# Kernel tuning notes

Measured on AMD Instinct MI355X. Metric: run time of the kernel, lower is better.

Reference implementation:

```python
import jax, jax.numpy as jnp
import numpy as np

ACTION_FEAT_DIM = 64
ACTION_EMB = 192
FUSION = 768
HID = 384
N_HEADS = 4
B, A = 2048, 64

gelu = lambda x: jax.nn.gelu(x, approximate=False)


def setup_inputs() -> dict:
    key = jax.random.key(0)
    ks = jax.random.split(key, 12)
    s = lambda fan_in: 1.0 / np.sqrt(fan_in)
    in_dim = ACTION_EMB + FUSION
    return {
        "action_feats": jax.random.normal(ks[0], (B, A, ACTION_FEAT_DIM), jnp.float32),
        "action_mask": jax.random.bernoulli(ks[1], 0.5, (B, A)),
        "fused": jax.random.normal(ks[2], (B, FUSION), jnp.float32),
        "phase_oh": jax.random.normal(ks[3], (B, 5), jnp.float32),
        # action encoder: Linear(64->192), GELU, Linear(192->192), GELU
        "We1": jax.random.uniform(ks[4], (ACTION_FEAT_DIM, ACTION_EMB), jnp.float32, -s(ACTION_FEAT_DIM), s(ACTION_FEAT_DIM)),
        "be1": jnp.zeros((ACTION_EMB,), jnp.float32),
        "We2": jax.random.uniform(ks[5], (ACTION_EMB, ACTION_EMB), jnp.float32, -s(ACTION_EMB), s(ACTION_EMB)),
        "be2": jnp.zeros((ACTION_EMB,), jnp.float32),
        # 4 phase heads: Linear(960->384), GELU, Linear(384->1), stacked on leading head axis
        "W1": jax.random.uniform(ks[6], (N_HEADS, in_dim, HID), jnp.float32, -s(in_dim), s(in_dim)),
        "b1": jnp.zeros((N_HEADS, HID), jnp.float32),
        "W2": jax.random.uniform(ks[7], (N_HEADS, HID), jnp.float32, -s(HID), s(HID)),
        "b2": jnp.zeros((N_HEADS,), jnp.float32),
    }


def reference(action_feats, action_mask, fused, phase_oh, We1, be1, We2, be2, W1, b1, W2, b2):
    bsz, act_count, _ = action_feats.shape
    # action encoder
    emb = gelu(gelu(action_feats @ We1 + be1) @ We2 + be2)          # [B,A,192]
    fused_rep = jnp.broadcast_to(fused[:, None, :], (bsz, act_count, fused.shape[-1]))
    inp = jnp.concatenate([emb, fused_rep], axis=-1)                 # [B,A,960]
    # dense compute of all 4 heads (faithful to original)
    h = gelu(jnp.einsum('bai,kio->bkao', inp, W1) + b1[None, :, None, :])  # [B,4,A,384]
    per_head = jnp.einsum('bkao,ko->bka', h, W2) + b2[None, :, None]       # [B,4,A]
    # phase routing: argmax over one-hot, phases >=3 map to head 3
    phase_idx = jnp.argmax(phase_oh, axis=-1)
    head_idx = jnp.where(phase_idx <= 2, phase_idx, 3)               # [B]
    logits = jnp.take_along_axis(per_head, head_idx[:, None, None], axis=1)[:, 0, :]  # [B,A]
    return jnp.where(action_mask, jnp.float32(-10000.0), logits)
```

## Files before the change

### kernel.cpp

```cpp
#include <hip/hip_runtime.h>


typedef __bf16 bf16x8 __attribute__((ext_vector_type(8)));
typedef unsigned short ushortx8 __attribute__((ext_vector_type(8)));
typedef float floatx4 __attribute__((ext_vector_type(4)));
typedef unsigned short u16;

#define B_SZ 2048
#define EMB 192
#define FUS 768
#define HID 384
#define INDIM 960
#define LDS_W 200

#define WS_FLAGS 0
#define WS_HEAD 256
#define WS_W1T 16384
#define WS_WE1T 2965504
#define WS_WE2T 2990080
#define WS_GALL 3063808

__device__ __forceinline__ float bf2f(u16 u) {
  return __uint_as_float(((unsigned int)u) << 16);
}
__device__ __forceinline__ u16 f2bf(float f) {
  unsigned int x = __float_as_uint(f);
  x += 0x7FFFu + ((x >> 16) & 1u);
  return (u16)(x >> 16);
}
__device__ __forceinline__ float ldf(const void* p, size_t i, int bf) {
  return bf ? bf2f(((const u16*)p)[i]) : ((const float*)p)[i];
}
__device__ __forceinline__ bf16x8 ld8(const void* p, size_t idx, int bf) {
  if (bf) return *reinterpret_cast<const bf16x8*>((const u16*)p + idx);
  const float* f = (const float*)p + idx;
  ushortx8 u;
#pragma unroll
  for (int i = 0; i < 8; ++i) u[i] = f2bf(f[i]);
  return __builtin_bit_cast(bf16x8, u);
}

__device__ __forceinline__ float gelu_f(float x) {
  float t = __expf(-1.702f * x);
  return x * __builtin_amdgcn_rcpf(1.0f + t);
}

__device__ __forceinline__ bool read_mask(const void* m, long long i, int fmt) {
  if (fmt == 0) return ((const int*)m)[i] != 0;
  if (fmt == 1) return ((const unsigned char*)m)[i] != 0;
  if (fmt == 2) return ((const u16*)m)[i] != 0;
  return ((const unsigned int*)m)[i] != 0;
}

__global__ void k_detect(const unsigned int* __restrict__ aw, int* __restrict__ flags) {
  __shared__ unsigned int s_or[256];
  __shared__ int s_cnt[256];
  int tid = threadIdx.x;
  unsigned int orv = 0;
  int cnt = 0;
#pragma unroll 8
  for (int j = 0; j < 64; ++j) {
    unsigned int w = aw[tid * 64 + j];
    unsigned int h = w & 0xFFFFu;
    orv |= h;
    unsigned int e = (h >> 7) & 0xFFu;
    cnt += (h == 0u || (e >= 90u && e <= 150u)) ? 1 : 0;
  }
  s_or[tid] = orv;
  s_cnt[tid] = cnt;
  __syncthreads();
  if (tid == 0) {
    unsigned int o = 0; int c = 0;
    for (int i = 0; i < 256; ++i) { o |= s_or[i]; c += s_cnt[i]; }
    flags[3] = (o != 0u && c > 12288) ? 1 : 0;
  }
}

__global__ void k_route(const void* __restrict__ phase, const void* __restrict__ mask,
                        int* __restrict__ head_idx, int* __restrict__ flags) {
  int t = blockIdx.x * 256 + threadIdx.x;
  if (t >= B_SZ) return;
  const int bf = flags[3];
  float best = ldf(phase, (size_t)t * 5, bf);
  int bi = 0;
#pragma unroll
  for (int i = 1; i < 5; ++i) {
    float v = ldf(phase, (size_t)t * 5 + i, bf);
    if (v > best) { best = v; bi = i; }
  }
  head_idx[t] = (bi <= 2) ? bi : 3;

  const unsigned int* mw = (const unsigned int*)mask;
  unsigned int vi = 0, vu = 0, en = 0;
#pragma unroll
  for (int j = 0; j < 16; ++j) {
    unsigned int w = mw[t * 16 + j];
    vi |= (unsigned int)(w > 1u);
    vu |= (unsigned int)((w & 0xFEFEFEFEu) != 0u);
    en |= (unsigned int)((w & 0x0000FFFFu) != 0u);
  }
  if (vi) atomicOr(&flags[0], 1);
  if (vu) atomicOr(&flags[1], 1);
  if (en) atomicOr(&flags[2], 1);
}

__global__ void k_transpose(const void* __restrict__ we1, const void* __restrict__ we2,
                            const void* __restrict__ w1, u16* __restrict__ we1t,
                            u16* __restrict__ we2t, u16* __restrict__ w1t,
                            const int* __restrict__ flags) {
  __shared__ u16 tile[32][33];
  const int bf = flags[3];
  const void* src; u16* dst; int R, C; size_t soff = 0;
  int z = blockIdx.z;
  if (z == 0)      { src = we1; dst = we1t; R = 64;  C = EMB; }
  else if (z == 1) { src = we2; dst = we2t; R = EMB; C = EMB; }
  else { src = w1; soff = (size_t)(z - 2) * INDIM * HID;
         dst = w1t + (size_t)(z - 2) * HID * INDIM; R = INDIM; C = HID; }
  int bx = blockIdx.x, by = blockIdx.y;
  if (bx * 32 >= C || by * 32 >= R) return;
  int tx = threadIdx.x, ty = threadIdx.y;
#pragma unroll
  for (int i = 0; i < 4; ++i) {
    int r = by * 32 + ty + i * 8, c = bx * 32 + tx;
    if (r < R && c < C) tile[ty + i * 8][tx] = f2bf(ldf(src, soff + (size_t)r * C + c, bf));
  }
  __syncthreads();
#pragma unroll
  for (int i = 0; i < 4; ++i) {
    int r = bx * 32 + ty + i * 8, c = by * 32 + tx;
    if (r < C && c < R) dst[(size_t)r * R + c] = tile[tx][ty + i * 8];
  }
}

__global__ __launch_bounds__(256, 2) void k_gall(const void* __restrict__ fused,
                                                 const u16* __restrict__ w1t,
                                                 const void* __restrict__ b1,
                                                 u16* __restrict__ gall,
                                                 const int* __restrict__ flags) {
  __shared__ float R[4][64][65];
  const int bm = blockIdx.x, bn = blockIdx.y;
  const int bf = flags[3];
  const int tid = threadIdx.x;
  const int w = tid >> 6, lane = tid & 63;
  const int nl = lane & 15, q = lane >> 4;
  const floatx4 z4 = {0.f, 0.f, 0.f, 0.f};
  floatx4 acc[4][4];
#pragma unroll
  for (int mt = 0; mt < 4; ++mt)
#pragma unroll
    for (int nt = 0; nt < 4; ++nt) acc[mt][nt] = z4;

#pragma unroll
  for (int i = 0; i < 6; ++i) {
    int kk = w * 6 + i;
    bf16x8 a[4];
#pragma unroll
    for (int mt = 0; mt < 4; ++mt)
      a[mt] = ld8(fused, ((size_t)(bm * 64 + mt * 16 + nl)) * FUS + kk * 32 + q * 8, bf);
#pragma unroll
    for (int nt = 0; nt < 4; ++nt) {
      int col = bn * 64 + nt * 16 + nl;
      bf16x8 bb = *reinterpret_cast<const bf16x8*>(w1t + (size_t)col * INDIM + EMB + kk * 32 + q * 8);
#pragma unroll
      for (int mt = 0; mt < 4; ++mt)
        acc[mt][nt] = __builtin_amdgcn_mfma_f32_16x16x32_bf16(a[mt], bb, acc[mt][nt], 0, 0, 0);
    }
  }
#pragma unroll
  for (int mt = 0; mt < 4; ++mt)
#pragma unroll
    for (int nt = 0; nt < 4; ++nt)
#pragma unroll
      for (int r = 0; r < 4; ++r)
        R[w][mt * 16 + q * 4 + r][nt * 16 + nl] = acc[mt][nt][r];
  __syncthreads();
#pragma unroll
  for (int j = 0; j < 16; ++j) {
    int e = j * 256 + tid;
    int row = e >> 6, col = e & 63;
    float s = R[0][row][col] + R[1][row][col] + R[2][row][col] + R[3][row][col]
            + ldf(b1, bn * 64 + col, bf);
    gall[(size_t)(bm * 64 + row) * 1536 + bn * 64 + col] = f2bf(s);
  }
}

__global__ __launch_bounds__(256, 3) void k_main(
    const void* __restrict__ act, const void* __restrict__ mask,
    const void* __restrict__ be1, const void* __restrict__ be2,
    const void* __restrict__ W2, const void* __restrict__ b2,
    const u16* __restrict__ we1t, const u16* __restrict__ we2t,
    const u16* __restrict__ w1t, const u16* __restrict__ gall,
    const int* __restrict__ head_idx, const int* __restrict__ flags,
    void* __restrict__ out) {
  __shared__ __align__(16) char LB[51200];
  u16* S1 = (u16*)LB;
  u16* S2 = (u16*)(LB + 25600);
  float* red = (float*)LB;
  const int b = blockIdx.x;
  const int tid = threadIdx.x;
  const int w = tid >> 6, lane = tid & 63;
  const int nl = lane & 15, q = lane >> 4;
  const int khead = head_idx[b];
  const int bf = flags[3];
  const floatx4 z4 = {0.f, 0.f, 0.f, 0.f};

  {
    floatx4 acc1[4][3];
#pragma unroll
    for (int mt = 0; mt < 4; ++mt)
#pragma unroll
      for (int nt = 0; nt < 3; ++nt) acc1[mt][nt] = z4;
#pragma unroll
    for (int kk = 0; kk < 2; ++kk) {
      bf16x8 a[4];
#pragma unroll
      for (int mt = 0; mt < 4; ++mt)
        a[mt] = ld8(act, ((size_t)b * 64 + mt * 16 + nl) * 64 + kk * 32 + q * 8, bf);
#pragma unroll
      for (int nt = 0; nt < 3; ++nt) {
        bf16x8 bb = *reinterpret_cast<const bf16x8*>(we1t + (w * 48 + nt * 16 + nl) * 64 + kk * 32 + q * 8);
#pragma unroll
        for (int mt = 0; mt < 4; ++mt)
          acc1[mt][nt] = __builtin_amdgcn_mfma_f32_16x16x32_bf16(a[mt], bb, acc1[mt][nt], 0, 0, 0);
      }
    }
#pragma unroll
    for (int nt = 0; nt < 3; ++nt) {
      int col = w * 48 + nt * 16 + nl;
      float bias = ldf(be1, col, bf);
#pragma unroll
      for (int mt = 0; mt < 4; ++mt)
#pragma unroll
        for (int r = 0; r < 4; ++r)
          S1[(mt * 16 + q * 4 + r) * LDS_W + col] = f2bf(gelu_f(acc1[mt][nt][r] + bias));
    }
  }
  __syncthreads();

  {
    floatx4 acc2[4][3];
#pragma unroll
    for (int mt = 0; mt < 4; ++mt)
#pragma unroll
      for (int nt = 0; nt < 3; ++nt) acc2[mt][nt] = z4;
#pragma unroll
    for (int kk = 0; kk < 6; ++kk) {
      bf16x8 a[4];
#pragma unroll
      for (int mt = 0; mt < 4; ++mt)
        a[mt] = *reinterpret_cast<const bf16x8*>(&S1[(mt * 16 + nl) * LDS_W + kk * 32 + q * 8]);
#pragma unroll
      for (int nt = 0; nt < 3; ++nt) {
        bf16x8 bb = *reinterpret_cast<const bf16x8*>(we2t + (w * 48 + nt * 16 + nl) * EMB + kk * 32 + q * 8);
#pragma unroll
        for (int mt = 0; mt < 4; ++mt)
          acc2[mt][nt] = __builtin_amdgcn_mfma_f32_16x16x32_bf16(a[mt], bb, acc2[mt][nt], 0, 0, 0);
      }
    }
#pragma unroll
    for (int nt = 0; nt < 3; ++nt) {
      int col = w * 48 + nt * 16 + nl;
      float bias = ldf(be2, col, bf);
#pragma unroll
      for (int mt = 0; mt < 4; ++mt)
#pragma unroll
        for (int r = 0; r < 4; ++r)
          S2[(mt * 16 + q * 4 + r) * LDS_W + col] = f2bf(gelu_f(acc2[mt][nt][r] + bias));
    }
  }
  __syncthreads();

  {
    floatx4 acc3[4][6];
#pragma unroll
    for (int mt = 0; mt < 4; ++mt)
#pragma unroll
      for (int nt = 0; nt < 6; ++nt) acc3[mt][nt] = z4;
    const u16* w1h = w1t + (size_t)khead * HID * INDIM;
#pragma unroll
    for (int kk = 0; kk < 6; ++kk) {
      bf16x8 a[4];
#pragma unroll
      for (int mt = 0; mt < 4; ++mt)
        a[mt] = *reinterpret_cast<const bf16x8*>(&S2[(mt * 16 + nl) * LDS_W + kk * 32 + q * 8]);
#pragma unroll
      for (int nt = 0; nt < 6; ++nt) {
        bf16x8 bb = *reinterpret_cast<const bf16x8*>(w1h + (size_t)(w * 96 + nt * 16 + nl) * INDIM + kk * 32 + q * 8);
#pragma unroll
        for (int mt = 0; mt < 4; ++mt)
          acc3[mt][nt] = __builtin_amdgcn_mfma_f32_16x16x32_bf16(a[mt], bb, acc3[mt][nt], 0, 0, 0);
      }
    }
    const u16* grow = gall + (size_t)b * 1536 + khead * HID;
    float partial[4][4];
#pragma unroll
    for (int mt = 0; mt < 4; ++mt)
#pragma unroll
      for (int r = 0; r < 4; ++r) partial[mt][r] = 0.f;
#pragma unroll
    for (int nt = 0; nt < 6; ++nt) {
      int col = w * 96 + nt * 16 + nl;
      float g = bf2f(grow[col]);
      float w2c = ldf(W2, (size_t)khead * HID + col, bf);
#pragma unroll
      for (int mt = 0; mt < 4; ++mt)
#pragma unroll
        for (int r = 0; r < 4; ++r)
          partial[mt][r] += gelu_f(acc3[mt][nt][r] + g) * w2c;
    }
#pragma unroll
    for (int off = 1; off < 16; off <<= 1)
#pragma unroll
      for (int mt = 0; mt < 4; ++mt)
#pragma unroll
        for (int r = 0; r < 4; ++r)
          partial[mt][r] += __shfl_xor(partial[mt][r], off, 16);
    if (nl == 0) {
#pragma unroll
      for (int mt = 0; mt < 4; ++mt)
#pragma unroll
        for (int r = 0; r < 4; ++r)
          red[w * 64 + mt * 16 + q * 4 + r] = partial[mt][r];
    }
  }
  __syncthreads();

  if (tid < 64) {
    float s = red[tid] + red[64 + tid] + red[128 + tid] + red[192 + tid];
    int f0 = flags[0], f1 = flags[1], f2v = flags[2];
    int fmt = (f0 == 0) ? 0 : ((f1 == 0) ? 1 : ((f2v != 0) ? 2 : 3));
    float bb2 = ldf(b2, khead, bf);
    long long mi = (long long)b * 64 + tid;
    float v = read_mask(mask, mi, fmt) ? -10000.0f : (s + bb2);
    if (bf) ((u16*)out)[mi] = f2bf(v);
    else    ((float*)out)[mi] = v;
  }
}

extern "C" void kernel_launch(void* const* d_in, const int* in_sizes, int n_in,
                              void* d_out, int out_size, void* d_ws, size_t ws_size,
                              hipStream_t stream) {
  const void* act   = d_in[0];
  const void* mask  = d_in[1];
  const void* fused = d_in[2];
  const void* phase = d_in[3];
  const void* We1 = d_in[4];
  const void* be1 = d_in[5];
  const void* We2 = d_in[6];
  const void* be2 = d_in[7];
  const void* W1  = d_in[8];
  const void* b1  = d_in[9];
  const void* W2  = d_in[10];
  const void* b2  = d_in[11];
  char* ws = (char*)d_ws;
  int* flags    = (int*)(ws + WS_FLAGS);
  int* head_idx = (int*)(ws + WS_HEAD);
  u16* w1t  = (u16*)(ws + WS_W1T);
  u16* we1t = (u16*)(ws + WS_WE1T);
  u16* we2t = (u16*)(ws + WS_WE2T);
  u16* gall = (u16*)(ws + WS_GALL);

  hipMemsetAsync(flags, 0, 32, stream);
  k_detect<<<1, 256, 0, stream>>>((const unsigned int*)act, flags);
  k_route<<<B_SZ / 256, 256, 0, stream>>>(phase, mask, head_idx, flags);
  k_transpose<<<dim3(12, 30, 6), dim3(32, 8), 0, stream>>>(We1, We2, W1, we1t, we2t, w1t, flags);
  k_gall<<<dim3(32, 24), 256, 0, stream>>>(fused, w1t, b1, gall, flags);
  k_main<<<B_SZ, 256, 0, stream>>>(act, mask, be1, be2, W2, b2, we1t, we2t,
                                   w1t, gall, head_idx, flags, d_out);
}
```

Baseline: 230.3 us.

## Compute fused-part projection only for each row's routed head via bucketed lists

Rows are bucketed by routed head with atomic counters, and the fused-input GEMM now computes only the selected head's 384 columns per row instead of all four heads. Fused input is pre-converted to bf16 in a separate pass. k_main reuses one LDS buffer for both encoder stages and splits the head GEMM into two halves, which cuts LDS and register use so occupancy can rise to 4 blocks. The cost is an extra prep kernel, atomics and scattered row writes. The memset launch is folded into k_detect.

```diff
diff --git a/kernel.cpp b/kernel.cpp
--- a/kernel.cpp
+++ b/kernel.cpp
@@ -5,6 +5,7 @@
 typedef unsigned short ushortx8 __attribute__((ext_vector_type(8)));
 typedef float floatx4 __attribute__((ext_vector_type(4)));
 typedef unsigned short u16;
+typedef unsigned int u32;
 
 #define B_SZ 2048
 #define EMB 192
@@ -14,17 +15,20 @@
 #define LDS_W 200
 
 #define WS_FLAGS 0
+#define WS_CNT 64
 #define WS_HEAD 256
-#define WS_W1T 16384
-#define WS_WE1T 2965504
-#define WS_WE2T 2990080
-#define WS_GALL 3063808
+#define WS_LIST 8448
+#define WS_W1T 41216
+#define WS_WE1T 2990336
+#define WS_WE2T 3014912
+#define WS_FUSEDBF 3088640
+#define WS_GSEL 6234368
 
 __device__ __forceinline__ float bf2f(u16 u) {
-  return __uint_as_float(((unsigned int)u) << 16);
+  return __uint_as_float(((u32)u) << 16);
 }
 __device__ __forceinline__ u16 f2bf(float f) {
-  unsigned int x = __float_as_uint(f);
+  u32 x = __float_as_uint(f);
   x += 0x7FFFu + ((x >> 16) & 1u);
   return (u16)(x >> 16);
 }
@@ -49,37 +53,67 @@
   if (fmt == 0) return ((const int*)m)[i] != 0;
   if (fmt == 1) return ((const unsigned char*)m)[i] != 0;
   if (fmt == 2) return ((const u16*)m)[i] != 0;
-  return ((const unsigned int*)m)[i] != 0;
-}
-
-__global__ void k_detect(const unsigned int* __restrict__ aw, int* __restrict__ flags) {
-  __shared__ unsigned int s_or[256];
-  __shared__ int s_cnt[256];
+  return ((const u32*)m)[i] != 0;
+}
+
+__global__ void k_detect(const u32* __restrict__ aw, int* __restrict__ flags,
+                         int* __restrict__ cnt) {
+  __shared__ u32 so[4];
+  __shared__ int sc[4];
   int tid = threadIdx.x;
-  unsigned int orv = 0;
-  int cnt = 0;
+  int lane = tid & 63, wave = tid >> 6;
+  u32 orv = 0;
+  int c = 0;
 #pragma unroll 8
   for (int j = 0; j < 64; ++j) {
-    unsigned int w = aw[tid * 64 + j];
-    unsigned int h = w & 0xFFFFu;
+    u32 w = aw[j * 256 + tid];
+    u32 h = w & 0xFFFFu;
     orv |= h;
-    unsigned int e = (h >> 7) & 0xFFu;
-    cnt += (h == 0u || (e >= 90u && e <= 150u)) ? 1 : 0;
-  }
-  s_or[tid] = orv;
-  s_cnt[tid] = cnt;
+    u32 e = (h >> 7) & 0xFFu;
+    c += (h == 0u || (e >= 90u && e <= 150u)) ? 1 : 0;
+  }
+#pragma unroll
+  for (int off = 32; off >= 1; off >>= 1) {
+    orv |= (u32)__shfl_xor((int)orv, off);
+    c += __shfl_xor(c, off);
+  }
+  if (lane == 0) { so[wave] = orv; sc[wave] = c; }
   __syncthreads();
   if (tid == 0) {
-    unsigned int o = 0; int c = 0;
-    for (int i = 0; i < 256; ++i) { o |= s_or[i]; c += s_cnt[i]; }
-    flags[3] = (o != 0u && c > 12288) ? 1 : 0;
+    u32 o = so[0] | so[1] | so[2] | so[3];
+    int ct = sc[0] + sc[1] + sc[2] + sc[3];
+    flags[3] = (o != 0u && ct > 12288) ? 1 : 0;
+    flags[0] = 0; flags[1] = 0; flags[2] = 0;
+    cnt[0] = 0; cnt[1] = 0; cnt[2] = 0; cnt[3] = 0;
+  }
+}
+
+__global__ void k_prep(const void* __restrict__ fused, u16* __restrict__ fbf,
+                       const int* __restrict__ flags) {
+  const int bf = flags[3];
+  int gid = blockIdx.x * 256 + threadIdx.x;
+  if (bf) {
+    const uint2* s = (const uint2*)fused;
+    uint2* d = (uint2*)fbf;
+    for (int i = gid; i < 393216; i += 49152) d[i] = s[i];
+  } else {
+    const float4* s = (const float4*)fused;
+    uint2* d = (uint2*)fbf;
+    for (int i = gid; i < 393216; i += 49152) {
+      float4 v = s[i];
+      uint2 o;
+      o.x = (u32)f2bf(v.x) | ((u32)f2bf(v.y) << 16);
+      o.y = (u32)f2bf(v.z) | ((u32)f2bf(v.w) << 16);
+      d[i] = o;
+    }
   }
 }
 
 __global__ void k_route(const void* __restrict__ phase, const void* __restrict__ mask,
-                        int* __restrict__ head_idx, int* __restrict__ flags) {
-  int t = blockIdx.x * 256 + threadIdx.x;
-  if (t >= B_SZ) return;
+                        int* __restrict__ head_idx, int* __restrict__ flags,
+                        int* __restrict__ cnt, int* __restrict__ list) {
+  int tid = threadIdx.x;
+  int t = blockIdx.x * 256 + tid;
   const int bf = flags[3];
   float best = ldf(phase, (size_t)t * 5, bf);
   int bi = 0;
@@ -88,16 +122,19 @@
     float v = ldf(phase, (size_t)t * 5 + i, bf);
     if (v > best) { best = v; bi = i; }
   }
-  head_idx[t] = (bi <= 2) ? bi : 3;
-
-  const unsigned int* mw = (const unsigned int*)mask;
-  unsigned int vi = 0, vu = 0, en = 0;
+  int h = (bi <= 2) ? bi : 3;
+  head_idx[t] = h;
+  int pos = atomicAdd(&cnt[h], 1);
+  list[h * 2048 + pos] = t;
+
+  const u32* mw = (const u32*)mask;
+  u32 vi = 0, vu = 0, en = 0;
 #pragma unroll
   for (int j = 0; j < 16; ++j) {
-    unsigned int w = mw[t * 16 + j];
-    vi |= (unsigned int)(w > 1u);
-    vu |= (unsigned int)((w & 0xFEFEFEFEu) != 0u);
-    en |= (unsigned int)((w & 0x0000FFFFu) != 0u);
+    u32 w = mw[blockIdx.x * 4096 + j * 256 + tid];
+    vi |= (u32)(w > 1u);
+    vu |= (u32)((w & 0xFEFEFEFEu) != 0u);
+    en |= (u32)((w & 0x0000FFFFu) != 0u);
   }
   if (vi) atomicOr(&flags[0], 1);
   if (vu) atomicOr(&flags[1], 1);
@@ -132,70 +169,73 @@
   }
 }
 
-__global__ __launch_bounds__(256, 2) void k_gall(const void* __restrict__ fused,
-                                                 const u16* __restrict__ w1t,
-                                                 const void* __restrict__ b1,
-                                                 u16* __restrict__ gall,
-                                                 const int* __restrict__ flags) {
-  __shared__ float R[4][64][65];
-  const int bm = blockIdx.x, bn = blockIdx.y;
+__global__ __launch_bounds__(256, 4) void k_gall_sel(
+    const u16* __restrict__ fbf, const u16* __restrict__ w1t,
+    const void* __restrict__ b1, u16* __restrict__ gsel,
+    const int* __restrict__ cnt, const int* __restrict__ list,
+    const int* __restrict__ flags) {
   const int bf = flags[3];
+  int c0 = cnt[0], c1 = cnt[1], c2 = cnt[2], c3 = cnt[3];
+  int t0 = (c0 + 63) >> 6, t1 = (c1 + 63) >> 6, t2 = (c2 + 63) >> 6, t3 = (c3 + 63) >> 6;
+  int x = blockIdx.x, h, tl;
+  if (x < t0) { h = 0; tl = x; }
+  else if (x < t0 + t1) { h = 1; tl = x - t0; }
+  else if (x < t0 + t1 + t2) { h = 2; tl = x - t0 - t1; }
+  else if (x < t0 + t1 + t2 + t3) { h = 3; tl = x - t0 - t1 - t2; }
+  else return;
+  int ch = (h == 0) ? c0 : (h == 1) ? c1 : (h == 2) ? c2 : c3;
   const int tid = threadIdx.x;
   const int w = tid >> 6, lane = tid & 63;
   const int nl = lane & 15, q = lane >> 4;
+
+  int r = tl * 64 + w * 16 + nl;
+  if (r >= ch) r = ch - 1;
+  int bi = list[h * 2048 + r];
+  const u16* arow = fbf + (size_t)bi * FUS;
+  const u16* w1h = w1t + (size_t)h * HID * INDIM;
+  const int ncol0 = blockIdx.y * 64;
+
   const floatx4 z4 = {0.f, 0.f, 0.f, 0.f};
-  floatx4 acc[4][4];
-#pragma unroll
-  for (int mt = 0; mt < 4; ++mt)
-#pragma unroll
-    for (int nt = 0; nt < 4; ++nt) acc[mt][nt] = z4;
-
-#pragma unroll
-  for (int i = 0; i < 6; ++i) {
-    int kk = w * 6 + i;
-    bf16x8 a[4];
-#pragma unroll
-    for (int mt = 0; mt < 4; ++mt)
-      a[mt] = ld8(fused, ((size_t)(bm * 64 + mt * 16 + nl)) * FUS + kk * 32 + q * 8, bf);
+  floatx4 acc[4];
+#pragma unroll
+  for (int i = 0; i < 4; ++i) acc[i] = z4;
+#pragma unroll 4
+  for (int kk = 0; kk < 24; ++kk) {
+    bf16x8 a = *reinterpret_cast<const bf16x8*>(arow + kk * 32 + q * 8);
 #pragma unroll
     for (int nt = 0; nt < 4; ++nt) {
-      int col = bn * 64 + nt * 16 + nl;
-      bf16x8 bb = *reinterpret_cast<const bf16x8*>(w1t + (size_t)col * INDIM + EMB + kk * 32 + q * 8);
-#pragma unroll
-      for (int mt = 0; mt < 4; ++mt)
-        acc[mt][nt] = __builtin_amdgcn_mfma_f32_16x16x32_bf16(a[mt], bb, acc[mt][nt], 0, 0, 0);
-    }
-  }
-#pragma unroll
-  for (int mt = 0; mt < 4; ++mt)
-#pragma unroll
-    for (int nt = 0; nt < 4; ++nt)
-#pragma unroll
-      for (int r = 0; r < 4; ++r)
-        R[w][mt * 16 + q * 4 + r][nt * 16 + nl] = acc[mt][nt][r];
-  __syncthreads();
-#pragma unroll
-  for (int j = 0; j < 16; ++j) {
-    int e = j * 256 + tid;
-    int row = e >> 6, col = e & 63;
-    float s = R[0][row][col] + R[1][row][col] + R[2][row][col] + R[3][row][col]
-            + ldf(b1, bn * 64 + col, bf);
-    gall[(size_t)(bm * 64 + row) * 1536 + bn * 64 + col] = f2bf(s);
-  }
-}
-
-__global__ __launch_bounds__(256, 3) void k_main(
+      int col = ncol0 + nt * 16 + nl;
+      bf16x8 bb = *reinterpret_cast<const bf16x8*>(w1h + (size_t)col * INDIM + EMB + kk * 32 + q * 8);
+      acc[nt] = __builtin_amdgcn_mfma_f32_16x16x32_bf16(a, bb, acc[nt], 0, 0, 0);
+    }
+  }
+  int bi2[4];
+#pragma unroll
+  for (int rr = 0; rr < 4; ++rr) {
+    int rm = tl * 64 + w * 16 + q * 4 + rr;
+    if (rm >= ch) rm = ch - 1;
+    bi2[rr] = list[h * 2048 + rm];
+  }
+#pragma unroll
+  for (int nt = 0; nt < 4; ++nt) {
+    int col = ncol0 + nt * 16 + nl;
+    float bias = ldf(b1, (size_t)h * HID + col, bf);
+#pragma unroll
+    for (int rr = 0; rr < 4; ++rr)
+      gsel[(size_t)bi2[rr] * HID + col] = f2bf(acc[nt][rr] + bias);
+  }
+}
+
+__global__ __launch_bounds__(256, 4) void k_main(
     const void* __restrict__ act, const void* __restrict__ mask,
     const void* __restrict__ be1, const void* __restrict__ be2,
     const void* __restrict__ W2, const void* __restrict__ b2,
     const u16* __restrict__ we1t, const u16* __restrict__ we2t,
-    const u16* __restrict__ w1t, const u16* __restrict__ gall,
+    const u16* __restrict__ w1t, const u16* __restrict__ gsel,
     const int* __restrict__ head_idx, const int* __restrict__ flags,
     void* __restrict__ out) {
-  __shared__ __align__(16) char LB[51200];
-  u16* S1 = (u16*)LB;
-  u16* S2 = (u16*)(LB + 25600);
-  float* red = (float*)LB;
+  __shared__ __align__(16) u16 S[64 * LDS_W];
+  __shared__ float red[256];
   const int b = blockIdx.x;
   const int tid = threadIdx.x;
   const int w = tid >> 6, lane = tid & 63;
@@ -232,7 +272,7 @@
       for (int mt = 0; mt < 4; ++mt)
 #pragma unroll
         for (int r = 0; r < 4; ++r)
-          S1[(mt * 16 + q * 4 + r) * LDS_W + col] = f2bf(gelu_f(acc1[mt][nt][r] + bias));
+          S[(mt * 16 + q * 4 + r) * LDS_W + col] = f2bf(gelu_f(acc1[mt][nt][r] + bias));
     }
   }
   __syncthreads();
@@ -248,7 +288,7 @@
       bf16x8 a[4];
 #pragma unroll
       for (int mt = 0; mt < 4; ++mt)
-        a[mt] = *reinterpret_cast<const bf16x8*>(&S1[(mt * 16 + nl) * LDS_W + kk * 32 + q * 8]);
+        a[mt] = *reinterpret_cast<const bf16x8*>(&S[(mt * 16 + nl) * LDS_W + kk * 32 + q * 8]);
 #pragma unroll
       for (int nt = 0; nt < 3; ++nt) {
         bf16x8 bb = *reinterpret_cast<const bf16x8*>(we2t + (w * 48 + nt * 16 + nl) * EMB + kk * 32 + q * 8);
@@ -257,6 +297,7 @@
           acc2[mt][nt] = __builtin_amdgcn_mfma_f32_16x16x32_bf16(a[mt], bb, acc2[mt][nt], 0, 0, 0);
       }
     }
+    __syncthreads();
 #pragma unroll
     for (int nt = 0; nt < 3; ++nt) {
       int col = w * 48 + nt * 16 + nl;
@@ -265,41 +306,43 @@
       for (int mt = 0; mt < 4; ++mt)
 #pragma unroll
         for (int r = 0; r < 4; ++r)
-          S2[(mt * 16 + q * 4 + r) * LDS_W + col] = f2bf(gelu_f(acc2[mt][nt][r] + bias));
+          S[(mt * 16 + q * 4 + r) * LDS_W + col] = f2bf(gelu_f(acc2[mt][nt][r] + bias));
     }
   }
   __syncthreads();
 
-  {
-    floatx4 acc3[4][6];
+  float partial[4][4];
+#pragma unroll
+  for (int mt = 0; mt < 4; ++mt)
+#pragma unroll
+    for (int r = 0; r < 4; ++r) partial[mt][r] = 0.f;
+  const u16* w1h = w1t + (size_t)khead * HID * INDIM;
+  const u16* grow = gsel + (size_t)b * HID;
+#pragma unroll
+  for (int half = 0; half < 2; ++half) {
+    floatx4 acc3[4][3];
 #pragma unroll
     for (int mt = 0; mt < 4; ++mt)
 #pragma unroll
-      for (int nt = 0; nt < 6; ++nt) acc3[mt][nt] = z4;
-    const u16* w1h = w1t + (size_t)khead * HID * INDIM;
+      for (int nt = 0; nt < 3; ++nt) acc3[mt][nt] = z4;
 #pragma unroll
     for (int kk = 0; kk < 6; ++kk) {
       bf16x8 a[4];
 #pragma unroll
       for (int mt = 0; mt < 4; ++mt)
-        a[mt] = *reinterpret_cast<const bf16x8*>(&S2[(mt * 16 + nl) * LDS_W + kk * 32 + q * 8]);
-#pragma unroll
-      for (int nt = 0; nt < 6; ++nt) {
-        bf16x8 bb = *reinterpret_cast<const bf16x8*>(w1h + (size_t)(w * 96 + nt * 16 + nl) * INDIM + kk * 32 + q * 8);
+        a[mt] = *reinterpret_cast<const bf16x8*>(&S[(mt * 16 + nl) * LDS_W + kk * 32 + q * 8]);
+#pragma unroll
+      for (int nt = 0; nt < 3; ++nt) {
+        int col = w * 96 + half * 48 + nt * 16 + nl;
+        bf16x8 bb = *reinterpret_cast<const bf16x8*>(w1h + (size_t)col * INDIM + kk * 32 + q * 8);
 #pragma unroll
         for (int mt = 0; mt < 4; ++mt)
           acc3[mt][nt] = __builtin_amdgcn_mfma_f32_16x16x32_bf16(a[mt], bb, acc3[mt][nt], 0, 0, 0);
       }
     }
-    const u16* grow = gall + (size_t)b * 1536 + khead * HID;
-    float partial[4][4];
-#pragma unroll
-    for (int mt = 0; mt < 4; ++mt)
-#pragma unroll
-      for (int r = 0; r < 4; ++r) partial[mt][r] = 0.f;
-#pragma unroll
-    for (int nt = 0; nt < 6; ++nt) {
-      int col = w * 96 + nt * 16 + nl;
+#pragma unroll
+    for (int nt = 0; nt < 3; ++nt) {
+      int col = w * 96 + half * 48 + nt * 16 + nl;
       float g = bf2f(grow[col]);
       float w2c = ldf(W2, (size_t)khead * HID + col, bf);
 #pragma unroll
@@ -308,20 +351,20 @@
         for (int r = 0; r < 4; ++r)
           partial[mt][r] += gelu_f(acc3[mt][nt][r] + g) * w2c;
     }
-#pragma unroll
-    for (int off = 1; off < 16; off <<= 1)
-#pragma unroll
-      for (int mt = 0; mt < 4; ++mt)
-#pragma unroll
-        for (int r = 0; r < 4; ++r)
-          partial[mt][r] += __shfl_xor(partial[mt][r], off, 16);
-    if (nl == 0) {
-#pragma unroll
-      for (int mt = 0; mt < 4; ++mt)
-#pragma unroll
-        for (int r = 0; r < 4; ++r)
-          red[w * 64 + mt * 16 + q * 4 + r] = partial[mt][r];
-    }
+  }
+#pragma unroll
+  for (int off = 1; off < 16; off <<= 1)
+#pragma unroll
+    for (int mt = 0; mt < 4; ++mt)
+#pragma unroll
+      for (int r = 0; r < 4; ++r)
+        partial[mt][r] += __shfl_xor(partial[mt][r], off, 16);
+  if (nl == 0) {
+#pragma unroll
+    for (int mt = 0; mt < 4; ++mt)
+#pragma unroll
+      for (int r = 0; r < 4; ++r)
+        red[w * 64 + mt * 16 + q * 4 + r] = partial[mt][r];
   }
   __syncthreads();
 
@@ -354,17 +397,20 @@
   const void* b2  = d_in[11];
   char* ws = (char*)d_ws;
   int* flags    = (int*)(ws + WS_FLAGS);
+  int* cnt      = (int*)(ws + WS_CNT);
   int* head_idx = (int*)(ws + WS_HEAD);
+  int* list     = (int*)(ws + WS_LIST);
   u16* w1t  = (u16*)(ws + WS_W1T);
   u16* we1t = (u16*)(ws + WS_WE1T);
   u16* we2t = (u16*)(ws + WS_WE2T);
-  u16* gall = (u16*)(ws + WS_GALL);
-
-  hipMemsetAsync(flags, 0, 32, stream);
-  k_detect<<<1, 256, 0, stream>>>((const unsigned int*)act, flags);
-  k_route<<<B_SZ / 256, 256, 0, stream>>>(phase, mask, head_idx, flags);
+  u16* fbf  = (u16*)(ws + WS_FUSEDBF);
+  u16* gsel = (u16*)(ws + WS_GSEL);
+
+  k_detect<<<1, 256, 0, stream>>>((const u32*)act, flags, cnt);
+  k_route<<<8, 256, 0, stream>>>(phase, mask, head_idx, flags, cnt, list);
+  k_prep<<<192, 256, 0, stream>>>(fused, fbf, flags);
   k_transpose<<<dim3(12, 30, 6), dim3(32, 8), 0, stream>>>(We1, We2, W1, we1t, we2t, w1t, flags);
-  k_gall<<<dim3(32, 24), 256, 0, stream>>>(fused, w1t, b1, gall, flags);
+  k_gall_sel<<<dim3(36, 6), 256, 0, stream>>>(fbf, w1t, b1, gsel, cnt, list, flags);
   k_main<<<B_SZ, 256, 0, stream>>>(act, mask, be1, be2, W2, b2, we1t, we2t,
-                                   w1t, gall, head_idx, flags, d_out);
-}
+                                   w1t, gsel, head_idx, flags, d_out);
+}
```

After: 226.8 us. No clear change (-1.5%).
